# Kernel tuning notes

Hardware: AMD Instinct MI355X
Metric: run time of the kernel (lower is better)

## Reference

```python
import jax, jax.numpy as jnp
import numpy as np

E, K, H, I = 8, 2, 1024, 3584  # num_experts, top_k, hidden, intermediate


def setup_inputs() -> dict:
    key = jax.random.key(0)
    k0, k1, k2, k3, k4 = jax.random.split(key, 5)
    scale = 0.02
    return {
        "hidden_states": jax.random.normal(k0, (2, 1024, H), dtype=jnp.float32),
        "w_gate": jax.random.normal(k1, (E, H), dtype=jnp.float32) * scale,  # gate Linear H->E
        "w1": jax.random.normal(k2, (E, I, H), dtype=jnp.float32) * scale,   # gate proj
        "w3": jax.random.normal(k3, (E, I, H), dtype=jnp.float32) * scale,   # up proj
        "w2": jax.random.normal(k4, (E, H, I), dtype=jnp.float32) * scale,   # down proj
    }


def reference(hidden_states, w_gate, w1, w3, w2):
    B, S, Hd = hidden_states.shape
    x = hidden_states.reshape(-1, Hd)                       # [T, H]
    logits = jnp.einsum('th,eh->te', x, w_gate)             # router logits [T, E]
    probs = jax.nn.softmax(logits, axis=-1)
    topw, topi = jax.lax.top_k(probs, K)                    # [T, K]
    topw = topw / jnp.sum(topw, axis=-1, keepdims=True)     # renormalize=True
    # dense combine weights [T, E] (zero off the top-k)
    comb = jnp.sum(jax.nn.one_hot(topi, E, dtype=x.dtype) * topw[..., None], axis=1)
    # SwiGLU experts (dense reference over all experts; math matches dispatch+combine)
    g = jnp.einsum('th,eih->eti', x, w1)                    # [E, T, I]
    u = jnp.einsum('th,eih->eti', x, w3)
    h = jax.nn.silu(g) * u
    out = jnp.einsum('eti,ehi->eth', h, w2)                 # [E, T, H]
    y = jnp.einsum('te,eth->th', comb, out)                 # weighted combine
    return y.reshape(B, S, Hd)
```

## Files before the change

kernel.cpp:

```cpp
#include <hip/hip_runtime.h>
#include <hip/hip_bf16.h>
#include <stdint.h>

#define NEXP 8
#define HD 1024
#define ID 3584
#define NTOK 2048
#define NSLOT 4096
#define SLOT_PAD 256
#define NSLOT_ALLOC (NSLOT + SLOT_PAD)
#define WN (NEXP * ID * HD)
#define KSPLIT 4
#define KLEN (ID / KSPLIT)

typedef unsigned short u16;
typedef __attribute__((ext_vector_type(8))) short s16x8;
typedef __attribute__((ext_vector_type(4))) short s16x4;
typedef __attribute__((ext_vector_type(4))) float f32x4;

__device__ __forceinline__ u16 f2bf(float f) {
    __hip_bfloat16 h = __float2bfloat16(f);
    union { __hip_bfloat16 h; u16 u; } v; v.h = h; return v.u;
}

__device__ __forceinline__ s16x8 cvt8(f32x4 a, f32x4 b) {
    s16x8 o;
    o[0]=(short)f2bf(a[0]); o[1]=(short)f2bf(a[1]); o[2]=(short)f2bf(a[2]); o[3]=(short)f2bf(a[3]);
    o[4]=(short)f2bf(b[0]); o[5]=(short)f2bf(b[1]); o[6]=(short)f2bf(b[2]); o[7]=(short)f2bf(b[3]);
    return o;
}

__device__ __forceinline__ void glds16(const void* g, void* l) {
    __builtin_amdgcn_global_load_lds((const __attribute__((address_space(1))) unsigned*)g,
                                     (__attribute__((address_space(3))) unsigned*)l, 16, 0, 0);
}

__global__ void init_kernel(int* __restrict__ counts) {
    if (threadIdx.x < 16) counts[threadIdx.x] = 0;
}

__global__ void router_kernel(const float* __restrict__ x, const float* __restrict__ wg,
                              int* __restrict__ topk_idx, float* __restrict__ topk_w,
                              int* __restrict__ counts) {
    int t = blockIdx.x;
    int lane = threadIdx.x;
    const float* xr = x + (size_t)t * HD;
    float acc[NEXP];
#pragma unroll
    for (int e = 0; e < NEXP; ++e) acc[e] = 0.f;
#pragma unroll
    for (int i = 0; i < HD / 256; ++i) {
        int h = i * 256 + lane * 4;
        f32x4 xv = *(const f32x4*)(xr + h);
#pragma unroll
        for (int e = 0; e < NEXP; ++e) {
            f32x4 wv = *(const f32x4*)(wg + e * HD + h);
            acc[e] += xv[0]*wv[0] + xv[1]*wv[1] + xv[2]*wv[2] + xv[3]*wv[3];
        }
    }
#pragma unroll
    for (int e = 0; e < NEXP; ++e) {
#pragma unroll
        for (int s = 32; s > 0; s >>= 1) acc[e] += __shfl_xor(acc[e], s, 64);
    }
    if (lane == 0) {
        int b0 = 0; float l0 = acc[0];
#pragma unroll
        for (int e = 1; e < NEXP; ++e) if (acc[e] > l0) { l0 = acc[e]; b0 = e; }
        int b1 = (b0 == 0) ? 1 : 0; float l1 = acc[b1];
#pragma unroll
        for (int e = 0; e < NEXP; ++e) {
            if (e == b0 || e == b1) continue;
            if (acc[e] > l1) { l1 = acc[e]; b1 = e; }
        }
        float w0 = 1.f / (1.f + expf(l1 - l0));
        float w1 = 1.f - w0;
        topk_idx[2 * t] = b0; topk_idx[2 * t + 1] = b1;
        topk_w[2 * t] = w0;  topk_w[2 * t + 1] = w1;
        atomicAdd(&counts[b0], 1);
        atomicAdd(&counts[b1], 1);
    }
}

__global__ void scan_kernel(const int* __restrict__ counts, int* __restrict__ offsets,
                            int* __restrict__ rows) {
    if (threadIdx.x == 0) {
        int off = 0;
#pragma unroll
        for (int e = 0; e < NEXP; ++e) { offsets[e] = off; off += counts[e]; }
    }
    if (threadIdx.x < SLOT_PAD) rows[NSLOT + threadIdx.x] = 0;
}

__global__ void assign_kernel(const int* __restrict__ topk_idx, const int* __restrict__ offsets,
                              int* __restrict__ counts2, int* __restrict__ rows,
                              int* __restrict__ slot_of) {
    int i = blockIdx.x * 256 + threadIdx.x;
    int e = topk_idx[i];
    int pos = atomicAdd(&counts2[e], 1);
    int slot = offsets[e] + pos;
    rows[slot] = i >> 1;
    slot_of[i] = slot;
}

__global__ __launch_bounds__(256)
void cvt3_kernel(const float* __restrict__ x, u16* __restrict__ xbf,
                 const float* __restrict__ w1, u16* __restrict__ w1bf,
                 const float* __restrict__ w3, u16* __restrict__ w3bf) {
    const int NX = NTOK * HD / 8, NW = WN / 8;
    int stride = gridDim.x * 256;
    for (int i = blockIdx.x * 256 + threadIdx.x; i < NX + 2 * NW; i += stride) {
        const float* s; u16* d; int j;
        if (i < NX)            { s = x;  d = xbf;  j = i; }
        else if (i < NX + NW)  { s = w1; d = w1bf; j = i - NX; }
        else                   { s = w3; d = w3bf; j = i - NX - NW; }
        f32x4 v0 = ((const f32x4*)s)[2 * j];
        f32x4 v1 = ((const f32x4*)s)[2 * j + 1];
        ((s16x8*)d)[j] = cvt8(v0, v1);
    }
}

#define G1_BLOCKS (NEXP * (NTOK / 128) * (ID / 128))
#define CVT2_BLOCKS 1024
__global__ __launch_bounds__(256, 2)
void gemm1_kernel(const u16* __restrict__ xbf, const u16* __restrict__ w1bf,
                  const u16* __restrict__ w3bf, const int* __restrict__ counts,
                  const int* __restrict__ offsets, const int* __restrict__ rows,
                  u16* __restrict__ hbuf,
                  const float* __restrict__ w2, u16* __restrict__ w2bf) {
    __shared__ u16 As[128][64];
    __shared__ u16 B1s[128][64];
    __shared__ u16 B3s[128][64];

    if (blockIdx.x >= G1_BLOCKS) {
        const int stride = CVT2_BLOCKS * 256;
        for (int i = (blockIdx.x - G1_BLOCKS) * 256 + threadIdx.x; i < WN / 8; i += stride) {
            f32x4 v0 = ((const f32x4*)w2)[2 * i];
            f32x4 v1 = ((const f32x4*)w2)[2 * i + 1];
            ((s16x8*)w2bf)[i] = cvt8(v0, v1);
        }
        return;
    }

    int bid = blockIdx.x;
    int gq = bid >> 7;
    int rm = bid & 127;
    int mt = rm >> 3;
    int g  = gq * 8 + (rm & 7);
    int e  = g / 28;
    int nt = g - e * 28;

    int n_e = counts[e];
    int m0 = mt * 128;
    if (m0 >= n_e) return;
    int off = offsets[e];
    int n0 = nt * 128;

    int tid = threadIdx.x;
    int lane = tid & 63;
    int wid = tid >> 6;

    int rsub = lane >> 3;
    int chunk = ((lane & 7) ^ rsub) * 8;
    int srow = wid * 32 + rsub;

    const u16 *srcA[4], *srcB1[4], *srcB3[4];
#pragma unroll
    for (int j = 0; j < 4; ++j) {
        int rl = srow + 8 * j;
        int tok = rows[off + m0 + rl];
        srcA[j]  = xbf  + (size_t)tok * HD + chunk;
        srcB1[j] = w1bf + ((size_t)e * ID + n0 + rl) * HD + chunk;
        srcB3[j] = w3bf + ((size_t)e * ID + n0 + rl) * HD + chunk;
    }

    f32x4 accg[4][4] = {}, accu[4][4] = {};
    int wm = (wid >> 1) * 64, wn = (wid & 1) * 64;
    int lr = lane & 15;
    int kk = lane >> 4;
    int ks0 = ((kk)     ^ (lr & 7)) * 8;
    int ks1 = ((4 + kk) ^ (lr & 7)) * 8;

    for (int k0 = 0; k0 < HD; k0 += 64) {
#pragma unroll
        for (int j = 0; j < 4; ++j) {
            glds16(srcA[j]  + k0, &As[wid * 32 + 8 * j][0]);
            glds16(srcB1[j] + k0, &B1s[wid * 32 + 8 * j][0]);
            glds16(srcB3[j] + k0, &B3s[wid * 32 + 8 * j][0]);
        }
        __syncthreads();
        s16x8 a[4], b1[4], b3[4];
#pragma unroll
        for (int f = 0; f < 4; ++f) {
            a[f]  = *(const s16x8*)&As[wm + f * 16 + lr][ks0];
            b1[f] = *(const s16x8*)&B1s[wn + f * 16 + lr][ks0];
            b3[f] = *(const s16x8*)&B3s[wn + f * 16 + lr][ks0];
        }
#pragma unroll
        for (int fm = 0; fm < 4; ++fm)
#pragma unroll
            for (int fn = 0; fn < 4; ++fn) {
                accg[fm][fn] = __builtin_amdgcn_mfma_f32_16x16x32_bf16(a[fm], b1[fn], accg[fm][fn], 0, 0, 0);
                accu[fm][fn] = __builtin_amdgcn_mfma_f32_16x16x32_bf16(a[fm], b3[fn], accu[fm][fn], 0, 0, 0);
            }
#pragma unroll
        for (int f = 0; f < 4; ++f) {
            a[f]  = *(const s16x8*)&As[wm + f * 16 + lr][ks1];
            b1[f] = *(const s16x8*)&B1s[wn + f * 16 + lr][ks1];
            b3[f] = *(const s16x8*)&B3s[wn + f * 16 + lr][ks1];
        }
#pragma unroll
        for (int fm = 0; fm < 4; ++fm)
#pragma unroll
            for (int fn = 0; fn < 4; ++fn) {
                accg[fm][fn] = __builtin_amdgcn_mfma_f32_16x16x32_bf16(a[fm], b1[fn], accg[fm][fn], 0, 0, 0);
                accu[fm][fn] = __builtin_amdgcn_mfma_f32_16x16x32_bf16(a[fm], b3[fn], accu[fm][fn], 0, 0, 0);
            }
        __syncthreads();
    }

    int lc = lane & 15;
    int lr4 = (lane >> 4) * 4;
#pragma unroll
    for (int fm = 0; fm < 4; ++fm) {
#pragma unroll
        for (int r = 0; r < 4; ++r) {
            int row = wm + fm * 16 + lr4 + r;
            if (m0 + row < n_e) {
                size_t base = (size_t)(off + m0 + row) * ID + n0 + wn;
#pragma unroll
                for (int fn = 0; fn < 4; ++fn) {
                    float g2 = accg[fm][fn][r];
                    float u = accu[fm][fn][r];
                    float hv = g2 * u / (1.f + expf(-g2));
                    hbuf[base + fn * 16 + lc] = f2bf(hv);
                }
            }
        }
    }
}

__global__ __launch_bounds__(256, 2)
void gemm2_kernel(const u16* __restrict__ hbuf, const u16* __restrict__ w2bf,
                  const int* __restrict__ counts, const int* __restrict__ offsets,
                  float* __restrict__ out2) {
    int bid = blockIdx.x;
    int e = bid & 7;
    int inner = bid >> 3;
    int mt = inner >> 5;
    int r2 = inner & 31;
    int nt = r2 >> 2;
    int ks = r2 & 3;

    int n_e = counts[e];
    int m0 = mt * 128;
    if (m0 >= n_e) return;
    int off = offsets[e];
    int n0 = nt * 128;
    int kbase = ks * KLEN;

    __shared__ u16 As[128][64];
    __shared__ u16 Bs[128][64];

    int tid = threadIdx.x;
    int lane = tid & 63;
    int wid = tid >> 6;

    int rsub = lane >> 3;
    int chunk = ((lane & 7) ^ rsub) * 8;
    int srow = wid * 32 + rsub;

    const u16 *srcA[4], *srcB[4];
#pragma unroll
    for (int j = 0; j < 4; ++j) {
        int rl = srow + 8 * j;
        srcA[j] = hbuf + (size_t)(off + m0 + rl) * ID + kbase + chunk;
        srcB[j] = w2bf + ((size_t)e * HD + n0 + rl) * ID + kbase + chunk;
    }

    f32x4 acc[4][4] = {};
    int wm = (wid >> 1) * 64, wn = (wid & 1) * 64;
    int lr = lane & 15;
    int kk = lane >> 4;
    int ks0 = ((kk)     ^ (lr & 7)) * 8;
    int ks1 = ((4 + kk) ^ (lr & 7)) * 8;

    for (int k0 = 0; k0 < KLEN; k0 += 64) {
#pragma unroll
        for (int j = 0; j < 4; ++j) {
            glds16(srcA[j] + k0, &As[wid * 32 + 8 * j][0]);
            glds16(srcB[j] + k0, &Bs[wid * 32 + 8 * j][0]);
        }
        __syncthreads();
        s16x8 a[4], b[4];
#pragma unroll
        for (int f = 0; f < 4; ++f) {
            a[f] = *(const s16x8*)&As[wm + f * 16 + lr][ks0];
            b[f] = *(const s16x8*)&Bs[wn + f * 16 + lr][ks0];
        }
#pragma unroll
        for (int fm = 0; fm < 4; ++fm)
#pragma unroll
            for (int fn = 0; fn < 4; ++fn)
                acc[fm][fn] = __builtin_amdgcn_mfma_f32_16x16x32_bf16(a[fm], b[fn], acc[fm][fn], 0, 0, 0);
#pragma unroll
        for (int f = 0; f < 4; ++f) {
            a[f] = *(const s16x8*)&As[wm + f * 16 + lr][ks1];
            b[f] = *(const s16x8*)&Bs[wn + f * 16 + lr][ks1];
        }
#pragma unroll
        for (int fm = 0; fm < 4; ++fm)
#pragma unroll
            for (int fn = 0; fn < 4; ++fn)
                acc[fm][fn] = __builtin_amdgcn_mfma_f32_16x16x32_bf16(a[fm], b[fn], acc[fm][fn], 0, 0, 0);
        __syncthreads();
    }

    float* outp = out2 + (size_t)ks * NSLOT_ALLOC * HD;
    int lc = lane & 15;
    int lr4 = (lane >> 4) * 4;
#pragma unroll
    for (int fm = 0; fm < 4; ++fm) {
#pragma unroll
        for (int r = 0; r < 4; ++r) {
            int row = wm + fm * 16 + lr4 + r;
            if (m0 + row < n_e) {
                float* dst = outp + (size_t)(off + m0 + row) * HD + n0 + wn;
#pragma unroll
                for (int fn = 0; fn < 4; ++fn)
                    dst[fn * 16 + lc] = acc[fm][fn][r];
            }
        }
    }
}

__global__ void combine_kernel(const float* __restrict__ out2, const int* __restrict__ slot_of,
                               const float* __restrict__ topk_w, float* __restrict__ y) {
    int i = blockIdx.x * 256 + threadIdx.x;
    int t = i >> 8;
    int c = i & 255;
    int s0 = slot_of[2 * t], s1 = slot_of[2 * t + 1];
    float w0 = topk_w[2 * t], w1 = topk_w[2 * t + 1];
    f32x4 o = {0.f, 0.f, 0.f, 0.f};
#pragma unroll
    for (int ks = 0; ks < KSPLIT; ++ks) {
        const float* p = out2 + (size_t)ks * NSLOT_ALLOC * HD;
        f32x4 a = ((const f32x4*)(p + (size_t)s0 * HD))[c];
        f32x4 b = ((const f32x4*)(p + (size_t)s1 * HD))[c];
#pragma unroll
        for (int j = 0; j < 4; ++j) o[j] += w0 * a[j] + w1 * b[j];
    }
    ((f32x4*)(y + (size_t)t * HD))[c] = o;
}

extern "C" void kernel_launch(void* const* d_in, const int* in_sizes, int n_in,
                              void* d_out, int out_size, void* d_ws, size_t ws_size,
                              hipStream_t stream) {
    (void)in_sizes; (void)n_in; (void)out_size; (void)ws_size;
    const float* x  = (const float*)d_in[0];
    const float* wg = (const float*)d_in[1];
    const float* w1 = (const float*)d_in[2];
    const float* w3 = (const float*)d_in[3];
    const float* w2 = (const float*)d_in[4];
    float* y = (float*)d_out;

    char* ws = (char*)d_ws;
    int*   counts   = (int*)(ws + 0);
    int*   counts2  = (int*)(ws + 32);
    int*   offsets  = (int*)(ws + 64);
    int*   topk_idx = (int*)(ws + 128);
    float* topk_w   = (float*)(ws + 128 + (size_t)NSLOT * 4);
    int*   rows     = (int*)(ws + 128 + (size_t)NSLOT * 8);
    int*   slot_of  = (int*)(ws + 128 + (size_t)NSLOT * 8 + (size_t)NSLOT_ALLOC * 4);
    size_t off_xbf = 128 + (size_t)NSLOT * 12 + (size_t)NSLOT_ALLOC * 4;
    off_xbf = (off_xbf + 255) & ~(size_t)255;
    u16* xbf = (u16*)(ws + off_xbf);
    size_t off_h = off_xbf + (size_t)NTOK * HD * 2;
    u16* hbuf = (u16*)(ws + off_h);
    size_t off_w1 = off_h + (size_t)NSLOT_ALLOC * ID * 2;
    u16* w1bf = (u16*)(ws + off_w1);
    size_t off_w3 = off_w1 + (size_t)WN * 2;
    u16* w3bf = (u16*)(ws + off_w3);
    size_t off_w2 = off_w3 + (size_t)WN * 2;
    u16* w2bf = (u16*)(ws + off_w2);
    size_t off_o2 = off_w2 + (size_t)WN * 2;
    float* out2 = (float*)(ws + off_o2);

    init_kernel<<<1, 64, 0, stream>>>(counts);
    router_kernel<<<NTOK, 64, 0, stream>>>(x, wg, topk_idx, topk_w, counts);
    scan_kernel<<<1, 256, 0, stream>>>(counts, offsets, rows);
    assign_kernel<<<NSLOT / 256, 256, 0, stream>>>(topk_idx, offsets, counts2, rows, slot_of);
    cvt3_kernel<<<4096, 256, 0, stream>>>(x, xbf, w1, w1bf, w3, w3bf);
    gemm1_kernel<<<G1_BLOCKS + CVT2_BLOCKS, 256, 0, stream>>>(xbf, w1bf, w3bf, counts, offsets, rows, hbuf, w2, w2bf);
    gemm2_kernel<<<NEXP * (NTOK / 128) * (HD / 128) * KSPLIT, 256, 0, stream>>>(hbuf, w2bf, counts, offsets, out2);
    combine_kernel<<<(NTOK * HD / 4) / 256, 256, 0, stream>>>(out2, slot_of, topk_w, y);
}
```

Before: 341.2 us.

## Fuse router into bf16 conversion kernel and drop split-K in down projection

Merges the router (now four tokens per 256-thread block) and the x/w1/w3 bf16 conversion into a single launch, so routing overlaps with the bandwidth-bound conversion and one kernel launch disappears. Removes the 4-way split-K in gemm2, so each block covers the full 3584-long K loop and writes a single partial output. The combine kernel then reads one partial per slot instead of four. This cuts partial-sum traffic but gives gemm2 a quarter as many blocks, which may leave CUs underused when experts get few tokens.

```diff
diff --git a/kernel.cpp b/kernel.cpp
--- a/kernel.cpp
+++ b/kernel.cpp
@@ -10,8 +10,6 @@
 #define SLOT_PAD 256
 #define NSLOT_ALLOC (NSLOT + SLOT_PAD)
 #define WN (NEXP * ID * HD)
-#define KSPLIT 4
-#define KLEN (ID / KSPLIT)
 
 typedef unsigned short u16;
 typedef __attribute__((ext_vector_type(8))) short s16x8;
@@ -39,11 +37,31 @@
     if (threadIdx.x < 16) counts[threadIdx.x] = 0;
 }
 
-__global__ void router_kernel(const float* __restrict__ x, const float* __restrict__ wg,
-                              int* __restrict__ topk_idx, float* __restrict__ topk_w,
-                              int* __restrict__ counts) {
-    int t = blockIdx.x;
-    int lane = threadIdx.x;
+#define RT_BLOCKS 512
+#define CVT3_BLOCKS 3072
+__global__ __launch_bounds__(256)
+void pre_kernel(const float* __restrict__ x, const float* __restrict__ wg,
+                int* __restrict__ topk_idx, float* __restrict__ topk_w,
+                int* __restrict__ counts,
+                u16* __restrict__ xbf,
+                const float* __restrict__ w1, u16* __restrict__ w1bf,
+                const float* __restrict__ w3, u16* __restrict__ w3bf) {
+    if (blockIdx.x >= RT_BLOCKS) {
+        const int NX = NTOK * HD / 8, NW = WN / 8;
+        const int stride = CVT3_BLOCKS * 256;
+        for (int i = (blockIdx.x - RT_BLOCKS) * 256 + threadIdx.x; i < NX + 2 * NW; i += stride) {
+            const float* s; u16* d; int j;
+            if (i < NX)            { s = x;  d = xbf;  j = i; }
+            else if (i < NX + NW)  { s = w1; d = w1bf; j = i - NX; }
+            else                   { s = w3; d = w3bf; j = i - NX - NW; }
+            f32x4 v0 = ((const f32x4*)s)[2 * j];
+            f32x4 v1 = ((const f32x4*)s)[2 * j + 1];
+            ((s16x8*)d)[j] = cvt8(v0, v1);
+        }
+        return;
+    }
+    int t = blockIdx.x * 4 + (threadIdx.x >> 6);
+    int lane = threadIdx.x & 63;
     const float* xr = x + (size_t)t * HD;
     float acc[NEXP];
 #pragma unroll
@@ -74,9 +92,9 @@
             if (acc[e] > l1) { l1 = acc[e]; b1 = e; }
         }
         float w0 = 1.f / (1.f + expf(l1 - l0));
-        float w1 = 1.f - w0;
+        float w1v = 1.f - w0;
         topk_idx[2 * t] = b0; topk_idx[2 * t + 1] = b1;
-        topk_w[2 * t] = w0;  topk_w[2 * t + 1] = w1;
+        topk_w[2 * t] = w0;  topk_w[2 * t + 1] = w1v;
         atomicAdd(&counts[b0], 1);
         atomicAdd(&counts[b1], 1);
     }
@@ -101,23 +119,6 @@
     int slot = offsets[e] + pos;
     rows[slot] = i >> 1;
     slot_of[i] = slot;
-}
-
-__global__ __launch_bounds__(256)
-void cvt3_kernel(const float* __restrict__ x, u16* __restrict__ xbf,
-                 const float* __restrict__ w1, u16* __restrict__ w1bf,
-                 const float* __restrict__ w3, u16* __restrict__ w3bf) {
-    const int NX = NTOK * HD / 8, NW = WN / 8;
-    int stride = gridDim.x * 256;
-    for (int i = blockIdx.x * 256 + threadIdx.x; i < NX + 2 * NW; i += stride) {
-        const float* s; u16* d; int j;
-        if (i < NX)            { s = x;  d = xbf;  j = i; }
-        else if (i < NX + NW)  { s = w1; d = w1bf; j = i - NX; }
-        else                   { s = w3; d = w3bf; j = i - NX - NW; }
-        f32x4 v0 = ((const f32x4*)s)[2 * j];
-        f32x4 v1 = ((const f32x4*)s)[2 * j + 1];
-        ((s16x8*)d)[j] = cvt8(v0, v1);
-    }
 }
 
 #define G1_BLOCKS (NEXP * (NTOK / 128) * (ID / 128))
@@ -247,17 +248,14 @@
     int bid = blockIdx.x;
     int e = bid & 7;
     int inner = bid >> 3;
-    int mt = inner >> 5;
-    int r2 = inner & 31;
-    int nt = r2 >> 2;
-    int ks = r2 & 3;
+    int mt = inner >> 3;
+    int nt = inner & 7;
 
     int n_e = counts[e];
     int m0 = mt * 128;
     if (m0 >= n_e) return;
     int off = offsets[e];
     int n0 = nt * 128;
-    int kbase = ks * KLEN;
 
     __shared__ u16 As[128][64];
     __shared__ u16 Bs[128][64];
@@ -274,8 +272,8 @@
 #pragma unroll
     for (int j = 0; j < 4; ++j) {
         int rl = srow + 8 * j;
-        srcA[j] = hbuf + (size_t)(off + m0 + rl) * ID + kbase + chunk;
-        srcB[j] = w2bf + ((size_t)e * HD + n0 + rl) * ID + kbase + chunk;
+        srcA[j] = hbuf + (size_t)(off + m0 + rl) * ID + chunk;
+        srcB[j] = w2bf + ((size_t)e * HD + n0 + rl) * ID + chunk;
     }
 
     f32x4 acc[4][4] = {};
@@ -285,7 +283,7 @@
     int ks0 = ((kk)     ^ (lr & 7)) * 8;
     int ks1 = ((4 + kk) ^ (lr & 7)) * 8;
 
-    for (int k0 = 0; k0 < KLEN; k0 += 64) {
+    for (int k0 = 0; k0 < ID; k0 += 64) {
 #pragma unroll
         for (int j = 0; j < 4; ++j) {
             glds16(srcA[j] + k0, &As[wid * 32 + 8 * j][0]);
@@ -316,7 +314,6 @@
         __syncthreads();
     }
 
-    float* outp = out2 + (size_t)ks * NSLOT_ALLOC * HD;
     int lc = lane & 15;
     int lr4 = (lane >> 4) * 4;
 #pragma unroll
@@ -325,7 +322,7 @@
         for (int r = 0; r < 4; ++r) {
             int row = wm + fm * 16 + lr4 + r;
             if (m0 + row < n_e) {
-                float* dst = outp + (size_t)(off + m0 + row) * HD + n0 + wn;
+                float* dst = out2 + (size_t)(off + m0 + row) * HD + n0 + wn;
 #pragma unroll
                 for (int fn = 0; fn < 4; ++fn)
                     dst[fn * 16 + lc] = acc[fm][fn][r];
@@ -341,15 +338,11 @@
     int c = i & 255;
     int s0 = slot_of[2 * t], s1 = slot_of[2 * t + 1];
     float w0 = topk_w[2 * t], w1 = topk_w[2 * t + 1];
-    f32x4 o = {0.f, 0.f, 0.f, 0.f};
-#pragma unroll
-    for (int ks = 0; ks < KSPLIT; ++ks) {
-        const float* p = out2 + (size_t)ks * NSLOT_ALLOC * HD;
-        f32x4 a = ((const f32x4*)(p + (size_t)s0 * HD))[c];
-        f32x4 b = ((const f32x4*)(p + (size_t)s1 * HD))[c];
-#pragma unroll
-        for (int j = 0; j < 4; ++j) o[j] += w0 * a[j] + w1 * b[j];
-    }
+    f32x4 a = ((const f32x4*)(out2 + (size_t)s0 * HD))[c];
+    f32x4 b = ((const f32x4*)(out2 + (size_t)s1 * HD))[c];
+    f32x4 o;
+#pragma unroll
+    for (int j = 0; j < 4; ++j) o[j] = w0 * a[j] + w1 * b[j];
     ((f32x4*)(y + (size_t)t * HD))[c] = o;
 }
 
@@ -387,11 +380,11 @@
     float* out2 = (float*)(ws + off_o2);
 
     init_kernel<<<1, 64, 0, stream>>>(counts);
-    router_kernel<<<NTOK, 64, 0, stream>>>(x, wg, topk_idx, topk_w, counts);
+    pre_kernel<<<RT_BLOCKS + CVT3_BLOCKS, 256, 0, stream>>>(x, wg, topk_idx, topk_w, counts,
+                                                            xbf, w1, w1bf, w3, w3bf);
     scan_kernel<<<1, 256, 0, stream>>>(counts, offsets, rows);
     assign_kernel<<<NSLOT / 256, 256, 0, stream>>>(topk_idx, offsets, counts2, rows, slot_of);
-    cvt3_kernel<<<4096, 256, 0, stream>>>(x, xbf, w1, w1bf, w3, w3bf);
     gemm1_kernel<<<G1_BLOCKS + CVT2_BLOCKS, 256, 0, stream>>>(xbf, w1bf, w3bf, counts, offsets, rows, hbuf, w2, w2bf);
-    gemm2_kernel<<<NEXP * (NTOK / 128) * (HD / 128) * KSPLIT, 256, 0, stream>>>(hbuf, w2bf, counts, offsets, out2);
+    gemm2_kernel<<<NEXP * (NTOK / 128) * (HD / 128), 256, 0, stream>>>(hbuf, w2bf, counts, offsets, out2);
     combine_kernel<<<(NTOK * HD / 4) / 256, 256, 0, stream>>>(out2, slot_of, topk_w, y);
 }
```

Result: faster. 334.3 us (-2.0%).
